# Optimization experiments

Hardware: AMD Instinct MI355X
Metric: run time of the kernel (lower is better)

## Reference

```python
import jax, jax.numpy as jnp
import numpy as np

N_NODES = 4096
N_EDGES = 16384
D_IN = 128
HID = 1024


def _linear_params(key, fan_in, fan_out):
    kw, kb = jax.random.split(key)
    bound = 1.0 / np.sqrt(fan_in)
    W = jax.random.uniform(kw, (fan_in, fan_out), jnp.float32, -bound, bound)
    b = jax.random.uniform(kb, (fan_out,), jnp.float32, -bound, bound)
    return W, b


def setup_inputs() -> dict:
    key = jax.random.key(0)
    ks = jax.random.split(key, 10)
    H = jax.random.normal(ks[0], (N_NODES, D_IN), jnp.float32)
    e = jax.random.uniform(ks[1], (N_NODES,), jnp.float32)
    # true incidence matrices: one-hot source/destination node per edge
    src = jax.random.randint(ks[2], (N_EDGES,), 0, N_NODES)
    dst = jax.random.randint(ks[3], (N_EDGES,), 0, N_NODES)
    Ro = jax.nn.one_hot(src, N_NODES, dtype=jnp.float32)  # [E, N]
    Ri = jax.nn.one_hot(dst, N_NODES, dtype=jnp.float32)  # [E, N]
    W1, b1 = _linear_params(ks[4], 3 * D_IN, HID)
    W2, b2 = _linear_params(ks[5], HID, HID)
    W3, b3 = _linear_params(ks[6], HID, HID // 2)
    W4, b4 = _linear_params(ks[7], HID // 2, HID // 4)
    W5, b5 = _linear_params(ks[8], HID // 4, 1)
    return {"H": H, "Ro": Ro, "Ri": Ri, "e": e,
            "W1": W1, "b1": b1, "W2": W2, "b2": b2, "W3": W3, "b3": b3,
            "W4": W4, "b4": b4, "W5": W5, "b5": b5}


def reference(H, Ro, Ri, e, W1, b1, W2, b2, W3, b3, W4, b4, W5, b5):
    eH = e[:, None] * H                      # [N, D]
    Ho = Ri.T @ (Ro @ eH)                    # aggregate over edges -> [N, D]
    Hi = Ro.T @ (Ri @ eH)                    # [N, D]
    x = jnp.concatenate([Ho, H, Hi], axis=1)  # [N, 3D]
    x = jnp.tanh(x @ W1 + b1)
    x = jnp.tanh(x @ W2 + b2)
    x = jnp.tanh(x @ W3 + b3)
    x = jnp.tanh(x @ W4 + b4)
    return jax.nn.sigmoid(x @ W5 + b5)       # [N, 1]
```

## Files before the change

kernel.cpp:

```cpp
#include <hip/hip_runtime.h>
#include <hip/hip_bf16.h>
#include <math.h>

#define N_NODES 4096
#define N_EDGES 16384
#define D_IN 128
#define HID 1024

typedef short s8v __attribute__((ext_vector_type(8)));
typedef float f4v __attribute__((ext_vector_type(4)));

__device__ __forceinline__ unsigned short f2b(float v) {
    union { float f; unsigned int u; } c; c.f = v;
    unsigned int u = c.u + 0x7fffu + ((c.u >> 16) & 1u);
    return (unsigned short)(u >> 16);
}
__device__ __forceinline__ void glds16(const unsigned short* g, unsigned short* l) {
    __builtin_amdgcn_global_load_lds(
        (const __attribute__((address_space(1))) void*)g,
        (__attribute__((address_space(3))) void*)l, 16, 0, 0);
}

__global__ void extract_scatter_wt(const float* __restrict__ Ro, const float* __restrict__ Ri,
                                   const float* __restrict__ H, const float* __restrict__ e,
                                   float* __restrict__ xf,
                                   const float* __restrict__ W1, unsigned short* __restrict__ wt1,
                                   const float* __restrict__ W2, unsigned short* __restrict__ wt2,
                                   const float* __restrict__ W3, unsigned short* __restrict__ wt3,
                                   const float* __restrict__ W4, unsigned short* __restrict__ wt4) {
    int b = blockIdx.x, t = threadIdx.x;
    if (b < 4096) {
        int edge = (b * 256 + t) >> 6;
        int l = t & 63;
        const f4v* ro4 = (const f4v*)(Ro + (size_t)edge * N_NODES);
        const f4v* ri4 = (const f4v*)(Ri + (size_t)edge * N_NODES);
        int src = -1, dst = -1;
        for (int g = 0; g < 4; ++g) {
            f4v va[4], vb[4];
            bool needA = (src < 0), needB = (dst < 0);
            if (needA) {
#pragma unroll
                for (int i = 0; i < 4; ++i)
                    va[i] = __builtin_nontemporal_load(&ro4[(g * 4 + i) * 64 + l]);
            }
            if (needB) {
#pragma unroll
                for (int i = 0; i < 4; ++i)
                    vb[i] = __builtin_nontemporal_load(&ri4[(g * 4 + i) * 64 + l]);
            }
            if (needA) {
#pragma unroll
                for (int i = 0; i < 4; ++i) {
                    if (src < 0) {
                        f4v v = va[i];
                        bool hit = (v.x != 0.0f) | (v.y != 0.0f) | (v.z != 0.0f) | (v.w != 0.0f);
                        unsigned long long m = __ballot(hit);
                        if (m) {
                            int fl = __ffsll((long long)m) - 1;
                            int idx = 0;
                            if (hit) idx = ((g * 4 + i) * 64 + l) * 4 +
                                           (v.x != 0.0f ? 0 : v.y != 0.0f ? 1 : v.z != 0.0f ? 2 : 3);
                            src = __shfl(idx, fl);
                        }
                    }
                }
            }
            if (needB) {
#pragma unroll
                for (int i = 0; i < 4; ++i) {
                    if (dst < 0) {
                        f4v v = vb[i];
                        bool hit = (v.x != 0.0f) | (v.y != 0.0f) | (v.z != 0.0f) | (v.w != 0.0f);
                        unsigned long long m = __ballot(hit);
                        if (m) {
                            int fl = __ffsll((long long)m) - 1;
                            int idx = 0;
                            if (hit) idx = ((g * 4 + i) * 64 + l) * 4 +
                                           (v.x != 0.0f ? 0 : v.y != 0.0f ? 1 : v.z != 0.0f ? 2 : 3);
                            dst = __shfl(idx, fl);
                        }
                    }
                }
            }
            if (src >= 0 && dst >= 0) break;
        }
        float es = e[src], ed = e[dst];
        if (l < 32) {
            int f = l * 4;
            float4 h = *(const float4*)(H + (size_t)src * 128 + f);
            float* o = xf + (size_t)dst * 256 + f;
            atomicAdd(o + 0, es * h.x); atomicAdd(o + 1, es * h.y);
            atomicAdd(o + 2, es * h.z); atomicAdd(o + 3, es * h.w);
        } else {
            int f = (l - 32) * 4;
            float4 h = *(const float4*)(H + (size_t)dst * 128 + f);
            float* o = xf + (size_t)src * 256 + 128 + f;
            atomicAdd(o + 0, ed * h.x); atomicAdd(o + 1, ed * h.y);
            atomicAdd(o + 2, ed * h.z); atomicAdd(o + 3, ed * h.w);
        }
        return;
    }
    int wb = b - 4096;
    const float* W; unsigned short* WT; int K, N, tb;
    if (wb < 384)       { W = W1; WT = wt1; K = 384;  N = 1024; tb = wb; }
    else if (wb < 1408) { W = W2; WT = wt2; K = 1024; N = 1024; tb = wb - 384; }
    else if (wb < 1920) { W = W3; WT = wt3; K = 1024; N = 512;  tb = wb - 1408; }
    else                { W = W4; WT = wt4; K = 512;  N = 256;  tb = wb - 1920; }
    __shared__ float tile[32][33];
    int ntx = N >> 5;
    int tk = tb / ntx, tn = tb - tk * ntx;
    int tr = t >> 5, tc = t & 31;
#pragma unroll
    for (int i = 0; i < 4; ++i)
        tile[tr + i * 8][tc] = W[(size_t)(tk * 32 + tr + i * 8) * N + tn * 32 + tc];
    __syncthreads();
#pragma unroll
    for (int i = 0; i < 4; ++i)
        WT[(size_t)(tn * 32 + tr + i * 8) * K + tk * 32 + tc] = f2b(tile[tc][tr + i * 8]);
}

#define L1_BM 128
#define L1_BN 64
__global__ __launch_bounds__(256)
void gemm1(const float* __restrict__ xf, const float* __restrict__ H,
           const unsigned short* __restrict__ BT, const float* __restrict__ bias,
           unsigned short* __restrict__ C) {
    constexpr int BK = 32, K = 384, N = HID;
    constexpr int MI = L1_BM / 32, NI = L1_BN / 32;
    __shared__ unsigned short As[L1_BM * BK];
    __shared__ unsigned short Bs[L1_BN * BK];
    int t = threadIdx.x;
    int l = t & 63, w = t >> 6;
    int wm = w >> 1, wn = w & 1;
    int q = l >> 4, r16 = l & 15;
    int m0 = blockIdx.y * L1_BM, n0 = blockIdx.x * L1_BN;

    f4v acc[MI][NI] = {};

    for (int k0 = 0; k0 < K; k0 += BK) {
        __syncthreads();
#pragma unroll
        for (int i = 0; i < 2; ++i) {
            int c = i * 256 + t;
            int row = c >> 2, ko = (c & 3) * 8;
            const float* sp;
            if (k0 < 128)      sp = xf + (size_t)(m0 + row) * 256 + k0 + ko;
            else if (k0 < 256) sp = H + (size_t)(m0 + row) * 128 + (k0 - 128) + ko;
            else               sp = xf + (size_t)(m0 + row) * 256 + (k0 - 128) + ko;
            float4 f0 = *(const float4*)sp, f1 = *(const float4*)(sp + 4);
            s8v pk;
            pk[0] = (short)f2b(f0.x); pk[1] = (short)f2b(f0.y);
            pk[2] = (short)f2b(f0.z); pk[3] = (short)f2b(f0.w);
            pk[4] = (short)f2b(f1.x); pk[5] = (short)f2b(f1.y);
            pk[6] = (short)f2b(f1.z); pk[7] = (short)f2b(f1.w);
            *(s8v*)&As[c * 8] = pk;
        }
        {
            int c = w * 64 + l;
            int row = c >> 2, ko = (c & 3) * 8;
            glds16(&BT[(size_t)(n0 + row) * K + k0 + ko], &Bs[c * 8]);
        }
        __syncthreads();
        s8v a[MI], b[NI];
#pragma unroll
        for (int mi = 0; mi < MI; ++mi)
            a[mi] = *(const s8v*)&As[(wm * (L1_BM / 2) + mi * 16 + r16) * BK + q * 8];
#pragma unroll
        for (int ni = 0; ni < NI; ++ni)
            b[ni] = *(const s8v*)&Bs[(wn * (L1_BN / 2) + ni * 16 + r16) * BK + q * 8];
#pragma unroll
        for (int mi = 0; mi < MI; ++mi)
#pragma unroll
            for (int ni = 0; ni < NI; ++ni)
                acc[mi][ni] = __builtin_amdgcn_mfma_f32_16x16x32_bf16(a[mi], b[ni], acc[mi][ni], 0, 0, 0);
    }
#pragma unroll
    for (int mi = 0; mi < MI; ++mi)
#pragma unroll
        for (int ni = 0; ni < NI; ++ni) {
            int col = n0 + wn * (L1_BN / 2) + ni * 16 + r16;
            float bv = bias[col];
#pragma unroll
            for (int r = 0; r < 4; ++r) {
                int row = m0 + wm * (L1_BM / 2) + mi * 16 + q * 4 + r;
                C[(size_t)row * N + col] = f2b(tanhf(acc[mi][ni][r] + bv));
            }
        }
}

template<int BM, int BN>
__global__ __launch_bounds__(256)
void gemm_tanh(const unsigned short* __restrict__ A, const unsigned short* __restrict__ BT,
               const float* __restrict__ bias, unsigned short* __restrict__ C,
               int M, int N, int K) {
    constexpr int BK = 32;
    constexpr int MI = BM / 32, NI = BN / 32;
    constexpr int AITER = BM / 64, BITER = BN / 64;
    __shared__ unsigned short As[BM * BK];
    __shared__ unsigned short Bs[BN * BK];
    int t = threadIdx.x;
    int l = t & 63, w = t >> 6;
    int wm = w >> 1, wn = w & 1;
    int q = l >> 4, r16 = l & 15;
    int m0 = blockIdx.y * BM, n0 = blockIdx.x * BN;

    f4v acc[MI][NI] = {};

    for (int k0 = 0; k0 < K; k0 += BK) {
        __syncthreads();
#pragma unroll
        for (int i = 0; i < AITER; ++i) {
            int c = (i * 4 + w) * 64 + l;
            int row = c >> 2, ko = (c & 3) * 8;
            glds16(&A[(size_t)(m0 + row) * K + k0 + ko], &As[c * 8]);
        }
#pragma unroll
        for (int i = 0; i < BITER; ++i) {
            int c = (i * 4 + w) * 64 + l;
            int row = c >> 2, ko = (c & 3) * 8;
            glds16(&BT[(size_t)(n0 + row) * K + k0 + ko], &Bs[c * 8]);
        }
        __syncthreads();
        s8v a[MI], b[NI];
#pragma unroll
        for (int mi = 0; mi < MI; ++mi)
            a[mi] = *(const s8v*)&As[(wm * (BM / 2) + mi * 16 + r16) * BK + q * 8];
#pragma unroll
        for (int ni = 0; ni < NI; ++ni)
            b[ni] = *(const s8v*)&Bs[(wn * (BN / 2) + ni * 16 + r16) * BK + q * 8];
#pragma unroll
        for (int mi = 0; mi < MI; ++mi)
#pragma unroll
            for (int ni = 0; ni < NI; ++ni)
                acc[mi][ni] = __builtin_amdgcn_mfma_f32_16x16x32_bf16(a[mi], b[ni], acc[mi][ni], 0, 0, 0);
    }
#pragma unroll
    for (int mi = 0; mi < MI; ++mi)
#pragma unroll
        for (int ni = 0; ni < NI; ++ni) {
            int col = n0 + wn * (BN / 2) + ni * 16 + r16;
            float bv = bias[col];
#pragma unroll
            for (int r = 0; r < 4; ++r) {
                int row = m0 + wm * (BM / 2) + mi * 16 + q * 4 + r;
                C[(size_t)row * N + col] = f2b(tanhf(acc[mi][ni][r] + bv));
            }
        }
}

__global__ __launch_bounds__(256)
void gemm45(const unsigned short* __restrict__ A, const unsigned short* __restrict__ BT,
            const float* __restrict__ b4, const float* __restrict__ W5,
            const float* __restrict__ b5, float* __restrict__ out) {
    constexpr int BK = 32, K = 512, NN = 256;
    constexpr int NI = 8;
    __shared__ unsigned short As[32 * BK];
    __shared__ unsigned short Bs[NN * BK];
    __shared__ float part[32][2];
    int t = threadIdx.x;
    int l = t & 63, w = t >> 6;
    int wm = w >> 1, wn = w & 1;
    int q = l >> 4, r16 = l & 15;
    int m0 = blockIdx.y * 32;

    f4v acc[NI] = {};

    for (int k0 = 0; k0 < K; k0 += BK) {
        __syncthreads();
        if (w < 2) {
            int c = w * 64 + l;
            int row = c >> 2, ko = (c & 3) * 8;
            glds16(&A[(size_t)(m0 + row) * K + k0 + ko], &As[c * 8]);
        }
#pragma unroll
        for (int i = 0; i < 4; ++i) {
            int c = (i * 4 + w) * 64 + l;
            int row = c >> 2, ko = (c & 3) * 8;
            glds16(&BT[(size_t)row * K + k0 + ko], &Bs[c * 8]);
        }
        __syncthreads();
        s8v a = *(const s8v*)&As[(wm * 16 + r16) * BK + q * 8];
        s8v b[NI];
#pragma unroll
        for (int ni = 0; ni < NI; ++ni)
            b[ni] = *(const s8v*)&Bs[(wn * 128 + ni * 16 + r16) * BK + q * 8];
#pragma unroll
        for (int ni = 0; ni < NI; ++ni)
            acc[ni] = __builtin_amdgcn_mfma_f32_16x16x32_bf16(a, b[ni], acc[ni], 0, 0, 0);
    }

    float partial[4] = {0.f, 0.f, 0.f, 0.f};
#pragma unroll
    for (int ni = 0; ni < NI; ++ni) {
        int col = wn * 128 + ni * 16 + r16;
        float bv = b4[col], wv = W5[col];
#pragma unroll
        for (int r = 0; r < 4; ++r)
            partial[r] += tanhf(acc[ni][r] + bv) * wv;
    }
#pragma unroll
    for (int off = 1; off < 16; off <<= 1)
#pragma unroll
        for (int r = 0; r < 4; ++r)
            partial[r] += __shfl_xor(partial[r], off);
    if (r16 == 0)
#pragma unroll
        for (int r = 0; r < 4; ++r)
            part[wm * 16 + q * 4 + r][wn] = partial[r];
    __syncthreads();
    if (t < 32) {
        float s = part[t][0] + part[t][1] + b5[0];
        out[m0 + t] = 1.0f / (1.0f + expf(-s));
    }
}

extern "C" void kernel_launch(void* const* d_in, const int* in_sizes, int n_in,
                              void* d_out, int out_size, void* d_ws, size_t ws_size,
                              hipStream_t stream) {
    const float* H  = (const float*)d_in[0];
    const float* Ro = (const float*)d_in[1];
    const float* Ri = (const float*)d_in[2];
    const float* e  = (const float*)d_in[3];
    const float* W1 = (const float*)d_in[4];  const float* b1 = (const float*)d_in[5];
    const float* W2 = (const float*)d_in[6];  const float* b2 = (const float*)d_in[7];
    const float* W3 = (const float*)d_in[8];  const float* b3 = (const float*)d_in[9];
    const float* W4 = (const float*)d_in[10]; const float* b4 = (const float*)d_in[11];
    const float* W5 = (const float*)d_in[12]; const float* b5 = (const float*)d_in[13];
    float* out = (float*)d_out;

    char* p = (char*)d_ws;
    auto alloc = [&](size_t bytes) -> void* {
        void* r = (void*)p;
        p += (bytes + 255) & ~(size_t)255;
        return r;
    };
    float* xf = (float*)alloc((size_t)N_NODES * 256 * 4);
    unsigned short* h1  = (unsigned short*)alloc((size_t)N_NODES * HID * 2);
    unsigned short* h2  = (unsigned short*)alloc((size_t)N_NODES * HID * 2);
    unsigned short* h3  = (unsigned short*)alloc((size_t)N_NODES * (HID / 2) * 2);
    unsigned short* wt1 = (unsigned short*)alloc((size_t)HID * 384 * 2);
    unsigned short* wt2 = (unsigned short*)alloc((size_t)HID * HID * 2);
    unsigned short* wt3 = (unsigned short*)alloc((size_t)(HID / 2) * HID * 2);
    unsigned short* wt4 = (unsigned short*)alloc((size_t)(HID / 4) * (HID / 2) * 2);

    extract_scatter_wt<<<4096 + 2048, 256, 0, stream>>>(Ro, Ri, H, e, xf,
                                                        W1, wt1, W2, wt2, W3, wt3, W4, wt4);

    gemm1<<<dim3(HID / L1_BN, N_NODES / L1_BM), 256, 0, stream>>>(xf, H, wt1, b1, h1);
    gemm_tanh<128, 64><<<dim3(HID / 64, N_NODES / 128), 256, 0, stream>>>(h1, wt2, b2, h2, N_NODES, HID, HID);
    gemm_tanh<64, 64><<<dim3((HID / 2) / 64, N_NODES / 64), 256, 0, stream>>>(h2, wt3, b3, h3, N_NODES, HID / 2, HID);

    gemm45<<<dim3(1, N_NODES / 32), 256, 0, stream>>>(h3, wt4, b4, W5, b5, out);
}
```

Baseline: 565.4 us.

## Fuse all stages into one cooperative persistent kernel with grid syncs

Replaces the five separate kernel launches with a single cooperative kernel of 512 blocks that runs the edge scan/scatter, weight transpose and the four GEMM stages in turn, separated by grid.sync barriers. The aim is to remove per-launch overhead and the gaps between kernels. Each block now handles several scan and transpose units in a loop, and the work split of the original launches is kept. If the cooperative launch fails, it falls back to five regular launches. In exchange, the grid is limited to co-resident blocks, and a single block with slow edges holds up every block at each barrier.

```diff
diff --git a/kernel.cpp b/kernel.cpp
--- a/kernel.cpp
+++ b/kernel.cpp
@@ -1,14 +1,18 @@
 #include <hip/hip_runtime.h>
+#include <hip/hip_cooperative_groups.h>
 #include <hip/hip_bf16.h>
 #include <math.h>
 
+namespace cg = cooperative_groups;
+
 #define N_NODES 4096
 #define N_EDGES 16384
-#define D_IN 128
 #define HID 1024
 
 typedef short s8v __attribute__((ext_vector_type(8)));
 typedef float f4v __attribute__((ext_vector_type(4)));
+
+#define SMEM_BYTES 18944
 
 __device__ __forceinline__ unsigned short f2b(float v) {
     union { float f; unsigned int u; } c; c.f = v;
@@ -21,92 +25,91 @@
         (__attribute__((address_space(3))) void*)l, 16, 0, 0);
 }
 
-__global__ void extract_scatter_wt(const float* __restrict__ Ro, const float* __restrict__ Ri,
-                                   const float* __restrict__ H, const float* __restrict__ e,
-                                   float* __restrict__ xf,
-                                   const float* __restrict__ W1, unsigned short* __restrict__ wt1,
-                                   const float* __restrict__ W2, unsigned short* __restrict__ wt2,
-                                   const float* __restrict__ W3, unsigned short* __restrict__ wt3,
-                                   const float* __restrict__ W4, unsigned short* __restrict__ wt4) {
-    int b = blockIdx.x, t = threadIdx.x;
-    if (b < 4096) {
-        int edge = (b * 256 + t) >> 6;
-        int l = t & 63;
-        const f4v* ro4 = (const f4v*)(Ro + (size_t)edge * N_NODES);
-        const f4v* ri4 = (const f4v*)(Ri + (size_t)edge * N_NODES);
-        int src = -1, dst = -1;
-        for (int g = 0; g < 4; ++g) {
-            f4v va[4], vb[4];
-            bool needA = (src < 0), needB = (dst < 0);
-            if (needA) {
-#pragma unroll
-                for (int i = 0; i < 4; ++i)
-                    va[i] = __builtin_nontemporal_load(&ro4[(g * 4 + i) * 64 + l]);
-            }
-            if (needB) {
-#pragma unroll
-                for (int i = 0; i < 4; ++i)
-                    vb[i] = __builtin_nontemporal_load(&ri4[(g * 4 + i) * 64 + l]);
-            }
-            if (needA) {
-#pragma unroll
-                for (int i = 0; i < 4; ++i) {
-                    if (src < 0) {
-                        f4v v = va[i];
-                        bool hit = (v.x != 0.0f) | (v.y != 0.0f) | (v.z != 0.0f) | (v.w != 0.0f);
-                        unsigned long long m = __ballot(hit);
-                        if (m) {
-                            int fl = __ffsll((long long)m) - 1;
-                            int idx = 0;
-                            if (hit) idx = ((g * 4 + i) * 64 + l) * 4 +
-                                           (v.x != 0.0f ? 0 : v.y != 0.0f ? 1 : v.z != 0.0f ? 2 : 3);
-                            src = __shfl(idx, fl);
-                        }
+__device__ __forceinline__ void scan_unit(int eb, int t,
+                                          const float* __restrict__ Ro, const float* __restrict__ Ri,
+                                          const float* __restrict__ H, const float* __restrict__ e,
+                                          float* __restrict__ xf) {
+    int w = t >> 6, l = t & 63;
+    int edge = eb * 4 + w;
+    const f4v* ro4 = (const f4v*)(Ro + (size_t)edge * N_NODES);
+    const f4v* ri4 = (const f4v*)(Ri + (size_t)edge * N_NODES);
+    int src = -1, dst = -1;
+    for (int g = 0; g < 4; ++g) {
+        f4v va[4], vb[4];
+        bool needA = (src < 0), needB = (dst < 0);
+        if (needA) {
+#pragma unroll
+            for (int i = 0; i < 4; ++i)
+                va[i] = __builtin_nontemporal_load(&ro4[(g * 4 + i) * 64 + l]);
+        }
+        if (needB) {
+#pragma unroll
+            for (int i = 0; i < 4; ++i)
+                vb[i] = __builtin_nontemporal_load(&ri4[(g * 4 + i) * 64 + l]);
+        }
+        if (needA) {
+#pragma unroll
+            for (int i = 0; i < 4; ++i) {
+                if (src < 0) {
+                    f4v v = va[i];
+                    bool hit = (v.x != 0.0f) | (v.y != 0.0f) | (v.z != 0.0f) | (v.w != 0.0f);
+                    unsigned long long m = __ballot(hit);
+                    if (m) {
+                        int fl = __ffsll((long long)m) - 1;
+                        int idx = 0;
+                        if (hit) idx = ((g * 4 + i) * 64 + l) * 4 +
+                                       (v.x != 0.0f ? 0 : v.y != 0.0f ? 1 : v.z != 0.0f ? 2 : 3);
+                        src = __shfl(idx, fl);
                     }
                 }
             }
-            if (needB) {
-#pragma unroll
-                for (int i = 0; i < 4; ++i) {
-                    if (dst < 0) {
-                        f4v v = vb[i];
-                        bool hit = (v.x != 0.0f) | (v.y != 0.0f) | (v.z != 0.0f) | (v.w != 0.0f);
-                        unsigned long long m = __ballot(hit);
-                        if (m) {
-                            int fl = __ffsll((long long)m) - 1;
-                            int idx = 0;
-                            if (hit) idx = ((g * 4 + i) * 64 + l) * 4 +
-                                           (v.x != 0.0f ? 0 : v.y != 0.0f ? 1 : v.z != 0.0f ? 2 : 3);
-                            dst = __shfl(idx, fl);
-                        }
+        }
+        if (needB) {
+#pragma unroll
+            for (int i = 0; i < 4; ++i) {
+                if (dst < 0) {
+                    f4v v = vb[i];
+                    bool hit = (v.x != 0.0f) | (v.y != 0.0f) | (v.z != 0.0f) | (v.w != 0.0f);
+                    unsigned long long m = __ballot(hit);
+                    if (m) {
+                        int fl = __ffsll((long long)m) - 1;
+                        int idx = 0;
+                        if (hit) idx = ((g * 4 + i) * 64 + l) * 4 +
+                                       (v.x != 0.0f ? 0 : v.y != 0.0f ? 1 : v.z != 0.0f ? 2 : 3);
+                        dst = __shfl(idx, fl);
                     }
                 }
             }
-            if (src >= 0 && dst >= 0) break;
-        }
-        float es = e[src], ed = e[dst];
-        if (l < 32) {
-            int f = l * 4;
-            float4 h = *(const float4*)(H + (size_t)src * 128 + f);
-            float* o = xf + (size_t)dst * 256 + f;
-            atomicAdd(o + 0, es * h.x); atomicAdd(o + 1, es * h.y);
-            atomicAdd(o + 2, es * h.z); atomicAdd(o + 3, es * h.w);
-        } else {
-            int f = (l - 32) * 4;
-            float4 h = *(const float4*)(H + (size_t)dst * 128 + f);
-            float* o = xf + (size_t)src * 256 + 128 + f;
-            atomicAdd(o + 0, ed * h.x); atomicAdd(o + 1, ed * h.y);
-            atomicAdd(o + 2, ed * h.z); atomicAdd(o + 3, ed * h.w);
-        }
-        return;
-    }
-    int wb = b - 4096;
+        }
+        if (src >= 0 && dst >= 0) break;
+    }
+    float es = e[src], ed = e[dst];
+    if (l < 32) {
+        int f = l * 4;
+        float4 h = *(const float4*)(H + (size_t)src * 128 + f);
+        float* o = xf + (size_t)dst * 256 + f;
+        atomicAdd(o + 0, es * h.x); atomicAdd(o + 1, es * h.y);
+        atomicAdd(o + 2, es * h.z); atomicAdd(o + 3, es * h.w);
+    } else {
+        int f = (l - 32) * 4;
+        float4 h = *(const float4*)(H + (size_t)dst * 128 + f);
+        float* o = xf + (size_t)src * 256 + 128 + f;
+        atomicAdd(o + 0, ed * h.x); atomicAdd(o + 1, ed * h.y);
+        atomicAdd(o + 2, ed * h.z); atomicAdd(o + 3, ed * h.w);
+    }
+}
+
+__device__ __forceinline__ void wt_unit(int wb, int t, char* smem,
+                                        const float* __restrict__ W1, unsigned short* __restrict__ wt1,
+                                        const float* __restrict__ W2, unsigned short* __restrict__ wt2,
+                                        const float* __restrict__ W3, unsigned short* __restrict__ wt3,
+                                        const float* __restrict__ W4, unsigned short* __restrict__ wt4) {
     const float* W; unsigned short* WT; int K, N, tb;
     if (wb < 384)       { W = W1; WT = wt1; K = 384;  N = 1024; tb = wb; }
     else if (wb < 1408) { W = W2; WT = wt2; K = 1024; N = 1024; tb = wb - 384; }
     else if (wb < 1920) { W = W3; WT = wt3; K = 1024; N = 512;  tb = wb - 1408; }
     else                { W = W4; WT = wt4; K = 512;  N = 256;  tb = wb - 1920; }
-    __shared__ float tile[32][33];
+    float (*tile)[33] = (float (*)[33])smem;
     int ntx = N >> 5;
     int tk = tb / ntx, tn = tb - tk * ntx;
     int tr = t >> 5, tc = t & 31;
@@ -117,23 +120,80 @@
 #pragma unroll
     for (int i = 0; i < 4; ++i)
         WT[(size_t)(tn * 32 + tr + i * 8) * K + tk * 32 + tc] = f2b(tile[tc][tr + i * 8]);
-}
-
-#define L1_BM 128
-#define L1_BN 64
-__global__ __launch_bounds__(256)
-void gemm1(const float* __restrict__ xf, const float* __restrict__ H,
-           const unsigned short* __restrict__ BT, const float* __restrict__ bias,
-           unsigned short* __restrict__ C) {
-    constexpr int BK = 32, K = 384, N = HID;
-    constexpr int MI = L1_BM / 32, NI = L1_BN / 32;
-    __shared__ unsigned short As[L1_BM * BK];
-    __shared__ unsigned short Bs[L1_BN * BK];
-    int t = threadIdx.x;
+    __syncthreads();
+}
+
+template<int BM, int BN>
+__device__ __forceinline__ void gemm_body(const unsigned short* __restrict__ A,
+                                          const unsigned short* __restrict__ BT,
+                                          const float* __restrict__ bias,
+                                          unsigned short* __restrict__ C,
+                                          int N, int K, int m0, int n0, char* smem, int t) {
+    constexpr int BK = 32;
+    constexpr int MI = BM / 32, NI = BN / 32;
+    constexpr int AITER = BM / 64, BITER = BN / 64;
+    unsigned short* As = (unsigned short*)smem;
+    unsigned short* Bs = As + BM * BK;
     int l = t & 63, w = t >> 6;
     int wm = w >> 1, wn = w & 1;
     int q = l >> 4, r16 = l & 15;
-    int m0 = blockIdx.y * L1_BM, n0 = blockIdx.x * L1_BN;
+
+    f4v acc[MI][NI] = {};
+
+    for (int k0 = 0; k0 < K; k0 += BK) {
+        __syncthreads();
+#pragma unroll
+        for (int i = 0; i < AITER; ++i) {
+            int c = (i * 4 + w) * 64 + l;
+            int row = c >> 2, ko = (c & 3) * 8;
+            glds16(&A[(size_t)(m0 + row) * K + k0 + ko], &As[c * 8]);
+        }
+#pragma unroll
+        for (int i = 0; i < BITER; ++i) {
+            int c = (i * 4 + w) * 64 + l;
+            int row = c >> 2, ko = (c & 3) * 8;
+            glds16(&BT[(size_t)(n0 + row) * K + k0 + ko], &Bs[c * 8]);
+        }
+        __syncthreads();
+        s8v a[MI], b[NI];
+#pragma unroll
+        for (int mi = 0; mi < MI; ++mi)
+            a[mi] = *(const s8v*)&As[(wm * (BM / 2) + mi * 16 + r16) * BK + q * 8];
+#pragma unroll
+        for (int ni = 0; ni < NI; ++ni)
+            b[ni] = *(const s8v*)&Bs[(wn * (BN / 2) + ni * 16 + r16) * BK + q * 8];
+#pragma unroll
+        for (int mi = 0; mi < MI; ++mi)
+#pragma unroll
+            for (int ni = 0; ni < NI; ++ni)
+                acc[mi][ni] = __builtin_amdgcn_mfma_f32_16x16x32_bf16(a[mi], b[ni], acc[mi][ni], 0, 0, 0);
+    }
+#pragma unroll
+    for (int mi = 0; mi < MI; ++mi)
+#pragma unroll
+        for (int ni = 0; ni < NI; ++ni) {
+            int col = n0 + wn * (BN / 2) + ni * 16 + r16;
+            float bv = bias[col];
+#pragma unroll
+            for (int r = 0; r < 4; ++r) {
+                int row = m0 + wm * (BM / 2) + mi * 16 + q * 4 + r;
+                C[(size_t)row * N + col] = f2b(tanhf(acc[mi][ni][r] + bv));
+            }
+        }
+}
+
+__device__ __forceinline__ void gemm1_body(const float* __restrict__ xf, const float* __restrict__ H,
+                                           const unsigned short* __restrict__ BT,
+                                           const float* __restrict__ bias,
+                                           unsigned short* __restrict__ C,
+                                           int m0, int n0, char* smem, int t) {
+    constexpr int BK = 32, K = 384, N = HID, BM = 128, BN = 64;
+    constexpr int MI = 4, NI = 2;
+    unsigned short* As = (unsigned short*)smem;
+    unsigned short* Bs = As + BM * BK;
+    int l = t & 63, w = t >> 6;
+    int wm = w >> 1, wn = w & 1;
+    int q = l >> 4, r16 = l & 15;
 
     f4v acc[MI][NI] = {};
 
@@ -164,10 +224,10 @@
         s8v a[MI], b[NI];
 #pragma unroll
         for (int mi = 0; mi < MI; ++mi)
-            a[mi] = *(const s8v*)&As[(wm * (L1_BM / 2) + mi * 16 + r16) * BK + q * 8];
+            a[mi] = *(const s8v*)&As[(wm * 64 + mi * 16 + r16) * BK + q * 8];
 #pragma unroll
         for (int ni = 0; ni < NI; ++ni)
-            b[ni] = *(const s8v*)&Bs[(wn * (L1_BN / 2) + ni * 16 + r16) * BK + q * 8];
+            b[ni] = *(const s8v*)&Bs[(wn * 32 + ni * 16 + r16) * BK + q * 8];
 #pragma unroll
         for (int mi = 0; mi < MI; ++mi)
 #pragma unroll
@@ -178,90 +238,29 @@
     for (int mi = 0; mi < MI; ++mi)
 #pragma unroll
         for (int ni = 0; ni < NI; ++ni) {
-            int col = n0 + wn * (L1_BN / 2) + ni * 16 + r16;
+            int col = n0 + wn * 32 + ni * 16 + r16;
             float bv = bias[col];
 #pragma unroll
             for (int r = 0; r < 4; ++r) {
-                int row = m0 + wm * (L1_BM / 2) + mi * 16 + q * 4 + r;
+                int row = m0 + wm * 64 + mi * 16 + q * 4 + r;
                 C[(size_t)row * N + col] = f2b(tanhf(acc[mi][ni][r] + bv));
             }
         }
 }
 
-template<int BM, int BN>
-__global__ __launch_bounds__(256)
-void gemm_tanh(const unsigned short* __restrict__ A, const unsigned short* __restrict__ BT,
-               const float* __restrict__ bias, unsigned short* __restrict__ C,
-               int M, int N, int K) {
-    constexpr int BK = 32;
-    constexpr int MI = BM / 32, NI = BN / 32;
-    constexpr int AITER = BM / 64, BITER = BN / 64;
-    __shared__ unsigned short As[BM * BK];
-    __shared__ unsigned short Bs[BN * BK];
-    int t = threadIdx.x;
+__device__ __forceinline__ void gemm45_body(const unsigned short* __restrict__ A,
+                                            const unsigned short* __restrict__ BT,
+                                            const float* __restrict__ b4, const float* __restrict__ W5,
+                                            const float* __restrict__ b5, float* __restrict__ out,
+                                            int m0, char* smem, int t) {
+    constexpr int BK = 32, K = 512;
+    constexpr int NI = 8;
+    unsigned short* As = (unsigned short*)smem;
+    unsigned short* Bs = As + 32 * BK;
+    float* part = (float*)(Bs + 256 * BK);
     int l = t & 63, w = t >> 6;
     int wm = w >> 1, wn = w & 1;
     int q = l >> 4, r16 = l & 15;
-    int m0 = blockIdx.y * BM, n0 = blockIdx.x * BN;
-
-    f4v acc[MI][NI] = {};
-
-    for (int k0 = 0; k0 < K; k0 += BK) {
-        __syncthreads();
-#pragma unroll
-        for (int i = 0; i < AITER; ++i) {
-            int c = (i * 4 + w) * 64 + l;
-            int row = c >> 2, ko = (c & 3) * 8;
-            glds16(&A[(size_t)(m0 + row) * K + k0 + ko], &As[c * 8]);
-        }
-#pragma unroll
-        for (int i = 0; i < BITER; ++i) {
-            int c = (i * 4 + w) * 64 + l;
-            int row = c >> 2, ko = (c & 3) * 8;
-            glds16(&BT[(size_t)(n0 + row) * K + k0 + ko], &Bs[c * 8]);
-        }
-        __syncthreads();
-        s8v a[MI], b[NI];
-#pragma unroll
-        for (int mi = 0; mi < MI; ++mi)
-            a[mi] = *(const s8v*)&As[(wm * (BM / 2) + mi * 16 + r16) * BK + q * 8];
-#pragma unroll
-        for (int ni = 0; ni < NI; ++ni)
-            b[ni] = *(const s8v*)&Bs[(wn * (BN / 2) + ni * 16 + r16) * BK + q * 8];
-#pragma unroll
-        for (int mi = 0; mi < MI; ++mi)
-#pragma unroll
-            for (int ni = 0; ni < NI; ++ni)
-                acc[mi][ni] = __builtin_amdgcn_mfma_f32_16x16x32_bf16(a[mi], b[ni], acc[mi][ni], 0, 0, 0);
-    }
-#pragma unroll
-    for (int mi = 0; mi < MI; ++mi)
-#pragma unroll
-        for (int ni = 0; ni < NI; ++ni) {
-            int col = n0 + wn * (BN / 2) + ni * 16 + r16;
-            float bv = bias[col];
-#pragma unroll
-            for (int r = 0; r < 4; ++r) {
-                int row = m0 + wm * (BM / 2) + mi * 16 + q * 4 + r;
-                C[(size_t)row * N + col] = f2b(tanhf(acc[mi][ni][r] + bv));
-            }
-        }
-}
-
-__global__ __launch_bounds__(256)
-void gemm45(const unsigned short* __restrict__ A, const unsigned short* __restrict__ BT,
-            const float* __restrict__ b4, const float* __restrict__ W5,
-            const float* __restrict__ b5, float* __restrict__ out) {
-    constexpr int BK = 32, K = 512, NN = 256;
-    constexpr int NI = 8;
-    __shared__ unsigned short As[32 * BK];
-    __shared__ unsigned short Bs[NN * BK];
-    __shared__ float part[32][2];
-    int t = threadIdx.x;
-    int l = t & 63, w = t >> 6;
-    int wm = w >> 1, wn = w & 1;
-    int q = l >> 4, r16 = l & 15;
-    int m0 = blockIdx.y * 32;
 
     f4v acc[NI] = {};
 
@@ -306,12 +305,80 @@
     if (r16 == 0)
 #pragma unroll
         for (int r = 0; r < 4; ++r)
-            part[wm * 16 + q * 4 + r][wn] = partial[r];
+            part[(wm * 16 + q * 4 + r) * 2 + wn] = partial[r];
     __syncthreads();
     if (t < 32) {
-        float s = part[t][0] + part[t][1] + b5[0];
+        float s = part[t * 2] + part[t * 2 + 1] + b5[0];
         out[m0 + t] = 1.0f / (1.0f + expf(-s));
     }
+}
+
+__global__ __launch_bounds__(256, 2)
+void mega(const float* Ro, const float* Ri, const float* H, const float* e,
+          const float* W1, const float* b1, const float* W2, const float* b2,
+          const float* W3, const float* b3, const float* W4, const float* b4,
+          const float* W5, const float* b5,
+          float* xf, unsigned short* h1, unsigned short* h2, unsigned short* h3,
+          unsigned short* wt1, unsigned short* wt2, unsigned short* wt3, unsigned short* wt4,
+          float* out) {
+    cg::grid_group grid = cg::this_grid();
+    __shared__ __align__(16) char smem[SMEM_BYTES];
+    int bid = blockIdx.x, t = threadIdx.x;
+
+    for (int u = 0; u < 8; ++u)
+        scan_unit(bid * 8 + u, t, Ro, Ri, H, e, xf);
+    for (int u = 0; u < 4; ++u)
+        wt_unit(bid * 4 + u, t, smem, W1, wt1, W2, wt2, W3, wt3, W4, wt4);
+    __threadfence();
+    grid.sync();
+
+    gemm1_body(xf, H, wt1, b1, h1, (bid >> 4) * 128, (bid & 15) * 64, smem, t);
+    __threadfence();
+    grid.sync();
+
+    gemm_body<128, 64>(h1, wt2, b2, h2, HID, HID, (bid >> 4) * 128, (bid & 15) * 64, smem, t);
+    __threadfence();
+    grid.sync();
+
+    gemm_body<64, 64>(h2, wt3, b3, h3, HID / 2, HID, (bid >> 3) * 64, (bid & 7) * 64, smem, t);
+    __threadfence();
+    grid.sync();
+
+    if (bid < 128)
+        gemm45_body(h3, wt4, b4, W5, b5, out, bid * 32, smem, t);
+}
+
+__global__ __launch_bounds__(256) void k_phaseA(const float* Ro, const float* Ri, const float* H,
+        const float* e, float* xf,
+        const float* W1, unsigned short* wt1, const float* W2, unsigned short* wt2,
+        const float* W3, unsigned short* wt3, const float* W4, unsigned short* wt4) {
+    __shared__ __align__(16) char smem[4352];
+    int bid = blockIdx.x, t = threadIdx.x;
+    for (int u = 0; u < 8; ++u) scan_unit(bid * 8 + u, t, Ro, Ri, H, e, xf);
+    for (int u = 0; u < 4; ++u) wt_unit(bid * 4 + u, t, smem, W1, wt1, W2, wt2, W3, wt3, W4, wt4);
+}
+__global__ __launch_bounds__(256) void k_gemm1(const float* xf, const float* H,
+        const unsigned short* wt1, const float* b1, unsigned short* h1) {
+    __shared__ __align__(16) char smem[12288];
+    int bid = blockIdx.x;
+    gemm1_body(xf, H, wt1, b1, h1, (bid >> 4) * 128, (bid & 15) * 64, smem, threadIdx.x);
+}
+__global__ __launch_bounds__(256) void k_gemm2(const unsigned short* h1, const unsigned short* wt2,
+        const float* b2, unsigned short* h2) {
+    __shared__ __align__(16) char smem[12288];
+    int bid = blockIdx.x;
+    gemm_body<128, 64>(h1, wt2, b2, h2, HID, HID, (bid >> 4) * 128, (bid & 15) * 64, smem, threadIdx.x);
+}
+__global__ __launch_bounds__(256) void k_gemm3(const unsigned short* h2, const unsigned short* wt3,
+        const float* b3, unsigned short* h3) {
+    __shared__ __align__(16) char smem[8192];
+    int bid = blockIdx.x;
+    gemm_body<64, 64>(h2, wt3, b3, h3, HID / 2, HID, (bid >> 3) * 64, (bid & 7) * 64, smem, threadIdx.x);
+}
+__global__ __launch_bounds__(256) void k_gemm45(const unsigned short* h3, const unsigned short* wt4,
+        const float* b4, const float* W5, const float* b5, float* out) {
+    __shared__ __align__(16) char smem[SMEM_BYTES];
+    gemm45_body(h3, wt4, b4, W5, b5, out, blockIdx.x * 32, smem, threadIdx.x);
 }
 
 extern "C" void kernel_launch(void* const* d_in, const int* in_sizes, int n_in,
@@ -343,12 +410,22 @@
     unsigned short* wt3 = (unsigned short*)alloc((size_t)(HID / 2) * HID * 2);
     unsigned short* wt4 = (unsigned short*)alloc((size_t)(HID / 4) * (HID / 2) * 2);
 
-    extract_scatter_wt<<<4096 + 2048, 256, 0, stream>>>(Ro, Ri, H, e, xf,
-                                                        W1, wt1, W2, wt2, W3, wt3, W4, wt4);
-
-    gemm1<<<dim3(HID / L1_BN, N_NODES / L1_BM), 256, 0, stream>>>(xf, H, wt1, b1, h1);
-    gemm_tanh<128, 64><<<dim3(HID / 64, N_NODES / 128), 256, 0, stream>>>(h1, wt2, b2, h2, N_NODES, HID, HID);
-    gemm_tanh<64, 64><<<dim3((HID / 2) / 64, N_NODES / 64), 256, 0, stream>>>(h2, wt3, b3, h3, N_NODES, HID / 2, HID);
-
-    gemm45<<<dim3(1, N_NODES / 32), 256, 0, stream>>>(h3, wt4, b4, W5, b5, out);
-}
+    void* args[] = {
+        (void*)&Ro, (void*)&Ri, (void*)&H, (void*)&e,
+        (void*)&W1, (void*)&b1, (void*)&W2, (void*)&b2,
+        (void*)&W3, (void*)&b3, (void*)&W4, (void*)&b4,
+        (void*)&W5, (void*)&b5,
+        (void*)&xf, (void*)&h1, (void*)&h2, (void*)&h3,
+        (void*)&wt1, (void*)&wt2, (void*)&wt3, (void*)&wt4,
+        (void*)&out
+    };
+    hipError_t err = hipLaunchCooperativeKernel((const void*)mega, dim3(512), dim3(256),
+                                                args, 0, stream);
+    if (err != hipSuccess) {
+        k_phaseA<<<512, 256, 0, stream>>>(Ro, Ri, H, e, xf, W1, wt1, W2, wt2, W3, wt3, W4, wt4);
+        k_gemm1 <<<512, 256, 0, stream>>>(xf, H, wt1, b1, h1);
+        k_gemm2 <<<512, 256, 0, stream>>>(h1, wt2, b2, h2);
+        k_gemm3 <<<512, 256, 0, stream>>>(h2, wt3, b3, h3);
+        k_gemm45<<<128, 256, 0, stream>>>(h3, wt4, b4, W5, b5, out);
+    }
+}
```

After: 1.032 ms. 82.6% more time.
